# Kernel tuning notes

Hardware: AMD Instinct MI355X
Metric: run time of the kernel (lower is better)

The kernel has to match this reference:

```python
import jax, jax.numpy as jnp
import numpy as np
from jax import lax

IN_CH = 512
OUT_CH = 512
KERNEL = 3
STYLE_DIM = 512
BATCH = 8
HW = 64
EPS = 1e-08
LR_MUL = 1.0


def setup_inputs() -> dict:
    key = jax.random.key(0)
    k1, k2, k3, k4 = jax.random.split(key, 4)
    x = jax.random.normal(k1, (BATCH, IN_CH, HW, HW), dtype=jnp.float32)
    style = jax.random.normal(k2, (BATCH, STYLE_DIM), dtype=jnp.float32)
    weight = jax.random.normal(k3, (1, OUT_CH, IN_CH, KERNEL, KERNEL), dtype=jnp.float32)
    mod_weight = jax.random.normal(k4, (IN_CH, STYLE_DIM), dtype=jnp.float32)
    mod_bias = jnp.ones((IN_CH,), dtype=jnp.float32)  # bias_init=1
    return {"x": x, "style": style, "weight": weight,
            "mod_weight": mod_weight, "mod_bias": mod_bias}


def reference(x, style, weight, mod_weight, mod_bias):
    batch, in_ch, h, w_dim = x.shape
    conv_scale = 1.0 / np.sqrt(in_ch * KERNEL * KERNEL)
    lin_scale = 1.0 / np.sqrt(STYLE_DIM) * LR_MUL

    # EqualizedLinear modulation: style -> per-channel scale, shape (B, in_ch)
    s = style @ (mod_weight * lin_scale).T + mod_bias * LR_MUL

    # Modulate: (B, out, in, k, k)
    w = conv_scale * weight * s[:, None, :, None, None]
    # Demodulate
    demod = lax.rsqrt(jnp.sum(w * w, axis=(2, 3, 4)) + EPS)  # (B, out)
    w = w * demod[:, :, None, None, None]

    pad = KERNEL // 2

    def conv_one(xi, wi):
        # xi: (in, H, W), wi: (out, in, k, k)
        return lax.conv_general_dilated(
            xi[None], wi, window_strides=(1, 1),
            padding=[(pad, pad), (pad, pad)],
            dimension_numbers=("NCHW", "OIHW", "NCHW"))[0]

    out = jax.vmap(conv_one)(x, w)  # (B, out, H, W)
    return out
```

## Files before the change

kernel.cpp:

```cpp
#include <hip/hip_runtime.h>
#include <hip/hip_bf16.h>
#include <cstdint>

#define IN_CH 512
#define OUT_CH 512
#define STYLE_DIM 512
#define BATCH 8
#define HW 64

typedef __bf16 bf16x8 __attribute__((ext_vector_type(8)));
typedef float f32x16 __attribute__((ext_vector_type(16)));

__device__ __forceinline__ void gload_lds16(const void* g, void* l) {
  __builtin_amdgcn_global_load_lds(
      (const __attribute__((address_space(1))) unsigned int*)g,
      (__attribute__((address_space(3))) unsigned int*)l,
      16, 0, 0);
}

#define WAITV(N) asm volatile("s_waitcnt vmcnt(" #N ")" ::: "memory")
#define BARRIER() do { asm volatile("" ::: "memory"); __builtin_amdgcn_s_barrier(); \
                       asm volatile("" ::: "memory"); } while (0)

__global__ void k_style(const float* __restrict__ style, const float* __restrict__ modw,
                        const float* __restrict__ modb, float* __restrict__ s_out) {
  __shared__ float st[BATCH * STYLE_DIM];
  const int tid = threadIdx.x;
  for (int i = tid; i < BATCH * STYLE_DIM; i += 256) st[i] = style[i];
  __syncthreads();
  const int ic = blockIdx.x * 4 + (tid >> 6);
  const int l = tid & 63;
  const float* mr = modw + (size_t)ic * STYLE_DIM + l * 8;
  float m[8];
  #pragma unroll
  for (int j = 0; j < 8; ++j) m[j] = mr[j];
  float accs[8];
  #pragma unroll
  for (int b = 0; b < 8; ++b) {
    const float* sb = st + b * STYLE_DIM + l * 8;
    float a = 0.f;
    #pragma unroll
    for (int j = 0; j < 8; ++j) a += m[j] * sb[j];
    accs[b] = a;
  }
  #pragma unroll
  for (int off = 32; off; off >>= 1) {
    #pragma unroll
    for (int b = 0; b < 8; ++b) accs[b] += __shfl_down(accs[b], off, 64);
  }
  if (l == 0) {
    #pragma unroll
    for (int b = 0; b < 8; ++b)
      s_out[b * IN_CH + ic] = accs[b] * 0.04419417382415922f + modb[ic];
  }
}

__global__ void k_wprep(const float* __restrict__ w, float* __restrict__ wsq,
                        __bf16* __restrict__ wb) {
  const int idx = blockIdx.x * 256 + threadIdx.x;
  const int oc = idx >> 9, ic = idx & 511;
  const float* p = w + ((size_t)oc * IN_CH + ic) * 9;
  const int icw = ic ^ ((oc & 7) << 3);
  float sum = 0.f;
  #pragma unroll
  for (int t = 0; t < 9; ++t) {
    float v = p[t];
    sum += v * v;
    wb[((size_t)(t * OUT_CH) + oc) * IN_CH + icw] = (__bf16)v;
  }
  wsq[oc * IN_CH + ic] = sum;
}

__global__ void k_demod(const float* __restrict__ s, const float* __restrict__ wsq,
                        float* __restrict__ scale) {
  const int oc = blockIdx.x;
  const int l = threadIdx.x;
  const float* wr = wsq + (size_t)oc * IN_CH + l * 8;
  float w8[8];
  #pragma unroll
  for (int j = 0; j < 8; ++j) w8[j] = wr[j];
  #pragma unroll
  for (int b = 0; b < 8; ++b) {
    const float* sb = s + b * IN_CH + l * 8;
    float acc = 0.f;
    #pragma unroll
    for (int j = 0; j < 8; ++j) { float sv = sb[j]; acc += sv * sv * w8[j]; }
    #pragma unroll
    for (int off = 32; off; off >>= 1) acc += __shfl_down(acc, off, 64);
    if (l == 0)
      scale[b * OUT_CH + oc] =
          rsqrtf(acc * (1.0f / 4608.0f) + 1e-8f) * 0.014731391274719732f;
  }
}

__global__ void k_xprep(const float* __restrict__ x, const float* __restrict__ s,
                        __bf16* __restrict__ xg) {
  const int b = blockIdx.x >> 6, y = blockIdx.x & 63;
  const int w = threadIdx.x >> 6, lane = threadIdx.x & 63;
  const float* sr = s + b * IN_CH;
  #pragma unroll
  for (int it = 0; it < 8; ++it) {
    const int ug = it * 8 + w;
    bf16x8 pk;
    #pragma unroll
    for (int j = 0; j < 8; ++j) {
      const int ic = ug * 8 + j;
      pk[j] = (__bf16)(x[(((size_t)(b * IN_CH) + ic) * HW + y) * HW + lane] * sr[ic]);
    }
    *(bf16x8*)(xg + ((((size_t)(b * 64 + ug) * HW + y) * HW + lane) * 8)) = pk;
  }
}

__global__ __launch_bounds__(512, 2) void k_conv(
    const __bf16* __restrict__ Wg,
    const __bf16* __restrict__ Xg,
    const float* __restrict__ scale,
    float* __restrict__ out)
{
  __shared__ __attribute__((aligned(16))) __bf16 Xs[6 * 66 * 64];
  __shared__ __attribute__((aligned(16))) __bf16 Wl[3][256 * 64];
  __shared__ __attribute__((aligned(16))) __bf16 Dump[4096];

  const int tid = threadIdx.x;
  const int lane = tid & 63;
  const int wid = tid >> 6;
  const int wm = wid >> 2;
  const int wn = wid & 3;
  const int ln31 = lane & 31;
  const int laneK = lane >> 5;

  const int bid0 = blockIdx.x;
  const int bid = (bid0 & 7) * 32 + (bid0 >> 3);
  const int octile = bid & 1;
  const int ptile = (bid >> 1) & 15;
  const int b = bid >> 5;
  const int oc0 = octile * 256;
  const int r0 = ptile * 4;

  auto stage_w = [&](int chunkv, int tapv, int bsel) {
    const int ic0 = chunkv * 64;
    #pragma unroll
    for (int i = 0; i < 4; ++i) {
      const int sidx = tid + 512 * i;
      const int oc = sidx >> 3, u = sidx & 7;
      gload_lds16(Wg + (((size_t)(tapv * OUT_CH) + oc0 + oc) * IN_CH + ic0 + u * 8),
                  &Wl[bsel][oc * 64 + u * 8]);
    }
  };
  auto stage_x = [&](int chunkv) {
    const int col = tid >> 3;
    const int u = tid & 7;
    const int ug = chunkv * 8 + (u ^ ((col + 1) & 7));
    #pragma unroll
    for (int j = 0; j < 6; ++j) {
      const int y = r0 - 1 + j;
      const bool ok = (y >= 0 && y < HW);
      const int yc = ok ? y : 0;
      void* dst = ok ? (void*)&Xs[(j * 66 + col + 1) * 64 + u * 8]
                     : (void*)&Dump[tid * 8];
      gload_lds16(Xg + ((((size_t)(b * 64 + ug) * HW + yc) * HW + col) * 8), dst);
    }
  };

  {
    float4 z = {0.f, 0.f, 0.f, 0.f};
    float4* p = (float4*)Xs;
    for (int i = tid; i < 6 * 66 * 64 / 8; i += 512) p[i] = z;
  }
  __syncthreads();
  stage_x(0);
  stage_w(0, 0, 0);
  stage_w(0, 1, 1);
  f32x16 acc[4][2] = {};
  const int akey8 = (ln31 & 7) << 3;
  const int kb = laneK * 8;

  int tap = 0, chunk = 0, wbuf = 0;

  for (int s = 0; s < 72; ++s) {
    if (s == 71) { WAITV(0); } else { WAITV(4); }
    BARRIER();

    const int dy = tap / 3 - 1, dx = tap % 3 - 1;
    const int xrow = wn + 1 + dy;
    const int col0 = ln31 + 1 + dx;
    const int bkey8 = (col0 & 7) << 3;
    const __bf16* __restrict__ wbase = &Wl[wbuf][(128 * wm + ln31) * 64];
    const __bf16* __restrict__ xb0 = &Xs[(xrow * 66 + col0) * 64];

    #pragma unroll
    for (int ks = 0; ks < 4; ++ks) {
      const int ael = (ks * 16 + kb) ^ akey8;
      const int bel = (ks * 16 + kb) ^ bkey8;
      bf16x8 av[4], bv[2];
      #pragma unroll
      for (int mf = 0; mf < 4; ++mf) av[mf] = *(const bf16x8*)(wbase + mf * 2048 + ael);
      bv[0] = *(const bf16x8*)(xb0 + bel);
      bv[1] = *(const bf16x8*)(xb0 + 32 * 64 + bel);
      __builtin_amdgcn_s_setprio(1);
      #pragma unroll
      for (int mf = 0; mf < 4; ++mf) {
        acc[mf][0] = __builtin_amdgcn_mfma_f32_32x32x16_bf16(av[mf], bv[0], acc[mf][0], 0, 0, 0);
        acc[mf][1] = __builtin_amdgcn_mfma_f32_32x32x16_bf16(av[mf], bv[1], acc[mf][1], 0, 0, 0);
      }
      __builtin_amdgcn_s_setprio(0);
    }

    const int wb2 = (wbuf >= 1) ? wbuf - 1 : wbuf + 2;
    if (tap == 8 && chunk < 7) {
      BARRIER();
      stage_x(chunk + 1);
      stage_w(chunk + 1, 1, wb2);
    } else if (s + 2 < 72) {
      int t2 = tap + 2, c2 = chunk;
      if (t2 >= 9) { t2 -= 9; ++c2; }
      stage_w(c2, t2, wb2);
    }

    if (++tap == 9) { tap = 0; ++chunk; }
    wbuf = (wbuf == 2) ? 0 : wbuf + 1;
  }

  const int y = r0 + wn;
  #pragma unroll
  for (int mf = 0; mf < 4; ++mf) {
    #pragma unroll
    for (int reg = 0; reg < 16; ++reg) {
      const int rowid = (reg & 3) + 8 * (reg >> 2) + 4 * laneK;
      const int oc = oc0 + 128 * wm + 32 * mf + rowid;
      const float sc = scale[b * OUT_CH + oc];
      float* op = out + (((size_t)(b * OUT_CH + oc) * HW + y) * HW) + ln31;
      op[0] = acc[mf][0][reg] * sc;
      op[32] = acc[mf][1][reg] * sc;
    }
  }
}

extern "C" void kernel_launch(void* const* d_in, const int* in_sizes, int n_in,
                              void* d_out, int out_size, void* d_ws, size_t ws_size,
                              hipStream_t stream) {
  const float* x      = (const float*)d_in[0];
  const float* style  = (const float*)d_in[1];
  const float* weight = (const float*)d_in[2];
  const float* modw   = (const float*)d_in[3];
  const float* modb   = (const float*)d_in[4];
  float* out = (float*)d_out;

  char* ws = (char*)d_ws;
  float*  s_buf = (float*)(ws + 0);
  float*  scale = (float*)(ws + 16384);
  float*  wsq   = (float*)(ws + 32768);
  __bf16* wb    = (__bf16*)(ws + 32768 + 1048576);
  __bf16* xg    = (__bf16*)(ws + 32768 + 1048576 + 9 * OUT_CH * IN_CH * 2);

  k_style<<<128, 256, 0, stream>>>(style, modw, modb, s_buf);
  k_wprep<<<1024, 256, 0, stream>>>(weight, wsq, wb);
  k_demod<<<512, 64, 0, stream>>>(s_buf, wsq, scale);
  k_xprep<<<BATCH * HW, 512, 0, stream>>>(x, s_buf, xg);
  k_conv<<<256, 512, 0, stream>>>(wb, xg, scale, out);
}
```

Measured before the change: 175.5 us.

## Fully unroll tap loop and software-pipeline LDS fragment reads against MFMAs

Restructures the conv main loop into an outer chunk loop with nine fully unrolled tap bodies. It precomputes the swizzled LDS addresses and double-buffers the A/B register fragments, so LDS reads for the next k-step or tap are issued while the current MFMAs run. This targets exposed LDS read latency and per-iteration index arithmetic. In exchange, every tap now waits with vmcnt(0) instead of vmcnt(4), which shortens how far global-to-LDS prefetch can run ahead. The extra fragment registers also raise register pressure.

```diff
diff --git a/kernel.cpp b/kernel.cpp
--- a/kernel.cpp
+++ b/kernel.cpp
@@ -171,54 +171,63 @@
   stage_x(0);
   stage_w(0, 0, 0);
   stage_w(0, 1, 1);
-  f32x16 acc[4][2] = {};
+
   const int akey8 = (ln31 & 7) << 3;
   const int kb = laneK * 8;
-
-  int tap = 0, chunk = 0, wbuf = 0;
-
-  for (int s = 0; s < 72; ++s) {
-    if (s == 71) { WAITV(0); } else { WAITV(4); }
-    BARRIER();
-
-    const int dy = tap / 3 - 1, dx = tap % 3 - 1;
-    const int xrow = wn + 1 + dy;
-    const int col0 = ln31 + 1 + dx;
-    const int bkey8 = (col0 & 7) << 3;
-    const __bf16* __restrict__ wbase = &Wl[wbuf][(128 * wm + ln31) * 64];
-    const __bf16* __restrict__ xb0 = &Xs[(xrow * 66 + col0) * 64];
-
-    #pragma unroll
-    for (int ks = 0; ks < 4; ++ks) {
-      const int ael = (ks * 16 + kb) ^ akey8;
-      const int bel = (ks * 16 + kb) ^ bkey8;
-      bf16x8 av[4], bv[2];
-      #pragma unroll
-      for (int mf = 0; mf < 4; ++mf) av[mf] = *(const bf16x8*)(wbase + mf * 2048 + ael);
-      bv[0] = *(const bf16x8*)(xb0 + bel);
-      bv[1] = *(const bf16x8*)(xb0 + 32 * 64 + bel);
-      __builtin_amdgcn_s_setprio(1);
-      #pragma unroll
-      for (int mf = 0; mf < 4; ++mf) {
-        acc[mf][0] = __builtin_amdgcn_mfma_f32_32x32x16_bf16(av[mf], bv[0], acc[mf][0], 0, 0, 0);
-        acc[mf][1] = __builtin_amdgcn_mfma_f32_32x32x16_bf16(av[mf], bv[1], acc[mf][1], 0, 0, 0);
-      }
-      __builtin_amdgcn_s_setprio(0);
-    }
-
-    const int wb2 = (wbuf >= 1) ? wbuf - 1 : wbuf + 2;
-    if (tap == 8 && chunk < 7) {
-      BARRIER();
-      stage_x(chunk + 1);
-      stage_w(chunk + 1, 1, wb2);
-    } else if (s + 2 < 72) {
-      int t2 = tap + 2, c2 = chunk;
-      if (t2 >= 9) { t2 -= 9; ++c2; }
-      stage_w(c2, t2, wb2);
-    }
-
-    if (++tap == 9) { tap = 0; ++chunk; }
-    wbuf = (wbuf == 2) ? 0 : wbuf + 1;
+  const __bf16* wbase[3];
+  #pragma unroll
+  for (int i = 0; i < 3; ++i) wbase[i] = &Wl[i][(128 * wm + ln31) * 64];
+  const __bf16* xbt[9];
+  #pragma unroll
+  for (int t = 0; t < 9; ++t) {
+    const int dy = t / 3 - 1, dx = t % 3 - 1;
+    xbt[t] = &Xs[((wn + 1 + dy) * 66 + (ln31 + 1 + dx)) * 64];
+  }
+  int aoffe[4];
+  #pragma unroll
+  for (int ks = 0; ks < 4; ++ks) aoffe[ks] = (ks * 16 + kb) ^ akey8;
+  int bele[3][4];
+  #pragma unroll
+  for (int dxi = 0; dxi < 3; ++dxi) {
+    const int bkey8 = ((ln31 + dxi) & 7) << 3;
+    #pragma unroll
+    for (int ks = 0; ks < 4; ++ks) bele[dxi][ks] = (ks * 16 + kb) ^ bkey8;
+  }
+
+  f32x16 acc[4][2] = {};
+  bf16x8 Aa[4], Ab[2], Ba[4], Bb[2];
+
+#define RDA(P, KS, BUF) { _Pragma("unroll") for (int mf = 0; mf < 4; ++mf) \
+    P##a[mf] = *(const bf16x8*)(wbase[BUF] + aoffe[KS] + mf * 2048); }
+#define RDB(P, TAP, KS) { const __bf16* p_ = xbt[TAP] + bele[(TAP) % 3][KS]; \
+    P##b[0] = *(const bf16x8*)p_; P##b[1] = *(const bf16x8*)(p_ + 2048); }
+#define MM(P) { __builtin_amdgcn_s_setprio(1); \
+    _Pragma("unroll") for (int mf = 0; mf < 4; ++mf) { \
+      acc[mf][0] = __builtin_amdgcn_mfma_f32_32x32x16_bf16(P##a[mf], P##b[0], acc[mf][0], 0, 0, 0); \
+      acc[mf][1] = __builtin_amdgcn_mfma_f32_32x32x16_bf16(P##a[mf], P##b[1], acc[mf][1], 0, 0, 0); } \
+    __builtin_amdgcn_s_setprio(0); }
+
+#define TAPBODY(T) { \
+    WAITV(0); BARRIER(); \
+    if ((T) == 0) { RDA(A, 0, 0) RDB(A, 0, 0) }             \
+    RDA(B, 1, (T) % 3) RDB(B, (T), 1)                        \
+    MM(A)                                                    \
+    if ((T) <= 6)      stage_w(c,     (T) + 2, ((T) + 2) % 3); \
+    else if (c < 7)    stage_w(c + 1, (T) - 7, ((T) + 2) % 3); \
+    RDA(A, 2, (T) % 3) RDB(A, (T), 2)                        \
+    MM(B)                                                    \
+    RDA(B, 3, (T) % 3) RDB(B, (T), 3)                        \
+    MM(A)                                                    \
+    if ((T) < 8) { RDA(A, 0, ((T) + 1) % 3) RDB(A, (T) + 1, 0) }   \
+    MM(B)                                                    \
+    if ((T) == 8) { BARRIER(); if (c < 7) stage_x(c + 1); } \
+  }
+
+  #pragma unroll 1
+  for (int c = 0; c < 8; ++c) {
+    TAPBODY(0) TAPBODY(1) TAPBODY(2)
+    TAPBODY(3) TAPBODY(4) TAPBODY(5)
+    TAPBODY(6) TAPBODY(7) TAPBODY(8)
   }
 
   const int y = r0 + wn;
```

Measured after the change: 191.6 us. +9.2%, slower.
